# Performance work log

Hardware: AMD Instinct MI355X
Metric: run time of the kernel (lower is better)

The kernel has to match this reference:

```python
import jax, jax.numpy as jnp
import numpy as np

N = 100000      # nodes
E = 1600000     # edges (avg degree 16)
IN_F, HID, OUT_F, NC = 384, 128, 64, 2
EPS = 1e-5
NEG_SLOPE = 0.01


def _layernorm(x, g, b):
    m = jnp.mean(x, axis=-1, keepdims=True)
    v = jnp.var(x, axis=-1, keepdims=True)
    return (x - m) * jax.lax.rsqrt(v + EPS) * g + b


def _graph_conv(x, edge_index, edge_weight, w_rel, b_rel, w_root):
    # PyG GraphConv: lin_rel(scatter_add(w_e * x[src] -> dst)) + lin_root(x)
    src, dst = edge_index[0], edge_index[1]
    msg = x[src] * edge_weight[:, None]                      # [E, C]
    agg = jax.ops.segment_sum(msg, dst, num_segments=x.shape[0])  # [N, C]
    return agg @ w_rel.T + b_rel + x @ w_root.T


def _xavier(key, shape):
    fan_in, fan_out = shape[1], shape[0]
    lim = float(np.sqrt(6.0 / (fan_in + fan_out)))
    return jax.random.uniform(key, shape, jnp.float32, -lim, lim)


def setup_inputs() -> dict:
    key = jax.random.key(0)
    ks = jax.random.split(key, 10)
    x = jax.random.normal(ks[0], (N, IN_F), jnp.float32)
    edge_index = jax.random.randint(ks[1], (2, E), 0, N, jnp.int64)
    edge_attr = jax.random.uniform(ks[2], (E,), jnp.float32)
    return {
        "x": x,
        "edge_index": edge_index,
        "edge_attr": edge_attr,
        "ln1_g": jnp.ones((IN_F,), jnp.float32),
        "ln1_b": jnp.zeros((IN_F,), jnp.float32),
        "fc1_w": _xavier(ks[3], (HID, IN_F)),
        "fc1_b": jnp.zeros((HID,), jnp.float32),
        "c1_wrel": _xavier(ks[4], (HID, HID)),
        "c1_brel": jnp.zeros((HID,), jnp.float32),
        "c1_wroot": _xavier(ks[5], (HID, HID)),
        "c2_wrel": _xavier(ks[6], (OUT_F, HID)),
        "c2_brel": jnp.zeros((OUT_F,), jnp.float32),
        "c2_wroot": _xavier(ks[7], (OUT_F, HID)),
        "ln2_g": jnp.ones((OUT_F,), jnp.float32),
        "ln2_b": jnp.zeros((OUT_F,), jnp.float32),
        "fc2_w": _xavier(ks[8], (NC, OUT_F)),
        "fc2_b": jnp.zeros((NC,), jnp.float32),
    }


def reference(x, edge_index, edge_attr,
              ln1_g, ln1_b, fc1_w, fc1_b,
              c1_wrel, c1_brel, c1_wroot,
              c2_wrel, c2_brel, c2_wroot,
              ln2_g, ln2_b, fc2_w, fc2_b):
    h = _layernorm(x, ln1_g, ln1_b) @ fc1_w.T + fc1_b          # [N, HID]
    h = _graph_conv(h, edge_index, edge_attr, c1_wrel, c1_brel, c1_wroot)
    h = jax.nn.leaky_relu(h, NEG_SLOPE)
    h = _graph_conv(h, edge_index, edge_attr, c2_wrel, c2_brel, c2_wroot)
    h = jax.nn.leaky_relu(h, NEG_SLOPE)                        # [N, OUT_F]
    out = _layernorm(h, ln2_g, ln2_b) @ fc2_w.T + fc2_b        # [N, NC]
    return out
```

## Files before the change

kernel.cpp:

```cpp
#include <hip/hip_runtime.h>
#include <hip/hip_bf16.h>

#define N_IN_F 384
#define N_HID  128
#define N_OUT  64

typedef unsigned short ushort_t;
typedef __attribute__((ext_vector_type(8))) short short8v;
typedef __attribute__((ext_vector_type(4))) float floatx4;

union U8 { uint4 v; unsigned short u[8]; };

__device__ __forceinline__ float bfu2f(unsigned short s){
    union { unsigned i; float f; } c; c.i = ((unsigned)s) << 16; return c.f;
}
__device__ __forceinline__ unsigned short f2bfu(float f){
    __hip_bfloat16 h = __float2bfloat16(f);
    union { __hip_bfloat16 h; unsigned short u; } c; c.h = h; return c.u;
}

__device__ __forceinline__ float loadS(const void* p, size_t i, int fm){
    return fm ? bfu2f(((const unsigned short*)p)[i]) : ((const float*)p)[i];
}

__global__ void k_detect_all(const int* __restrict__ ei, const unsigned* __restrict__ xw,
                             int* __restrict__ modep){
    int lane = threadIdx.x & 63;
    int zi = 0;
    if (lane < 32) zi = ei[2*lane + 1];
    int cnt = 0;
    #pragma unroll
    for (int q = 0; q < 8; q++){
        unsigned w = xw[lane*8 + q];
        unsigned elo = (w >> 7) & 0xff;
        cnt += (elo >= 118 && elo <= 134) ? 1 : 0;
    }
    #pragma unroll
    for (int m = 32; m; m >>= 1){ zi |= __shfl_xor(zi, m, 64); cnt += __shfl_xor(cnt, m, 64); }
    if (lane == 0 && blockIdx.x == 0){
        modep[0] = (zi == 0) ? 1 : 0;
        modep[1] = (cnt >= 256) ? 1 : 0;
    }
}

__device__ __forceinline__ int edge_src(const int* ei, int e, int i, int mode){
    return mode ? ei[2*(size_t)i] : ei[i];
}
__device__ __forceinline__ int edge_dst(const int* ei, int e, int i, int mode){
    return mode ? ei[2*(size_t)e + 2*(size_t)i] : ei[(size_t)e + i];
}

__global__ void k_hist(const int* __restrict__ ei, int e, int n, const int* __restrict__ modep,
                       int* __restrict__ deg, unsigned* __restrict__ rel){
    int i = blockIdx.x * 256 + threadIdx.x;
    if (i >= e) return;
    int mode = modep[0];
    int d = edge_dst(ei, e, i, mode);
    if ((unsigned)d >= (unsigned)n) return;
    rel[i] = (unsigned)atomicAdd(&deg[d], 1);
}

__global__ __launch_bounds__(1024) void k_blksum(
    const int* __restrict__ deg, int n, int* __restrict__ part)
{
    __shared__ int s[1024];
    int i = blockIdx.x * 1024 + threadIdx.x;
    s[threadIdx.x] = (i < n) ? deg[i] : 0;
    __syncthreads();
    for (int off = 512; off; off >>= 1){
        if (threadIdx.x < off) s[threadIdx.x] += s[threadIdx.x + off];
        __syncthreads();
    }
    if (threadIdx.x == 0) part[blockIdx.x] = s[0];
}

__global__ __launch_bounds__(128) void k_scanpart(
    int* __restrict__ part, int nb, int* __restrict__ rowoff, int n)
{
    __shared__ int s[128];
    int t = threadIdx.x;
    if (nb <= 128){
        int v = (t < nb) ? part[t] : 0;
        s[t] = v; __syncthreads();
        #pragma unroll
        for (int off = 1; off < 128; off <<= 1){
            int tmp = (t >= off) ? s[t - off] : 0;
            __syncthreads();
            s[t] += tmp;
            __syncthreads();
        }
        if (t < nb) part[t] = s[t] - v;
        if (t == 127) rowoff[n] = s[127];
    } else if (t == 0){
        int run = 0;
        for (int b = 0; b < nb; b++){ int tt = part[b]; part[b] = run; run += tt; }
        rowoff[n] = run;
    }
}

__global__ __launch_bounds__(1024) void k_scanblk(
    int* __restrict__ deg, const int* __restrict__ part, int n, int* __restrict__ rowoff)
{
    __shared__ int s[1024];
    int t = threadIdx.x;
    int i = blockIdx.x * 1024 + t;
    int v = (i < n) ? deg[i] : 0;
    s[t] = v; __syncthreads();
    for (int off = 1; off < 1024; off <<= 1){
        int tmp = (t >= off) ? s[t - off] : 0;
        __syncthreads();
        s[t] += tmp;
        __syncthreads();
    }
    if (i < n){
        int excl = s[t] - v + part[blockIdx.x];
        rowoff[i] = excl;
        deg[i]    = excl;
    }
}

__global__ void k_scatter(const int* __restrict__ ei, const void* __restrict__ ea,
                          int e, int n, const int* __restrict__ modep,
                          int* __restrict__ cursor, int2* __restrict__ colw)
{
    int i = blockIdx.x * 256 + threadIdx.x;
    if (i >= e) return;
    int mode = modep[0], fm = modep[1];
    int d = edge_dst(ei, e, i, mode);
    if ((unsigned)d >= (unsigned)n) return;
    int s = edge_src(ei, e, i, mode);
    if ((unsigned)s >= (unsigned)n) s = 0;
    int pos = atomicAdd(&cursor[d], 1);
    if ((unsigned)pos >= (unsigned)e) return;
    int2 pk; pk.x = s; pk.y = __float_as_int(loadS(ea, i, fm));
    colw[pos] = pk;
}

#define SC_CHUNK 2048
#define SC_BSHIFT 13
#define SC_MAXB 1024
__global__ __launch_bounds__(256) void k_scoarse(
    const int* __restrict__ ei, const void* __restrict__ ea,
    const unsigned* __restrict__ rel, const int* __restrict__ rowoff,
    const int* __restrict__ modep, int e, int n, int B,
    int4* __restrict__ tmp, int* __restrict__ off2)
{
    __shared__ int  hcnt[SC_MAXB];
    __shared__ int  hoff[SC_MAXB + 1];
    __shared__ int4 stage[SC_CHUNK];
    int t = threadIdx.x;
    int c = blockIdx.x;
    int chunk0 = c * SC_CHUNK;
    int mode = modep[0], fm = modep[1];

    for (int q = t; q < B; q += 256) hcnt[q] = 0;
    __syncthreads();

    int  pos[8], sv[8], wv[8];
    bool val[8];
    #pragma unroll
    for (int k = 0; k < 8; k++){
        int i = chunk0 + k*256 + t;
        val[k] = false;
        if (i < e){
            int d = edge_dst(ei, e, i, mode);
            if ((unsigned)d < (unsigned)n){
                int s = edge_src(ei, e, i, mode);
                if ((unsigned)s >= (unsigned)n) s = 0;
                int p = rowoff[d] + (int)rel[i];
                pos[k] = p; sv[k] = s; wv[k] = __float_as_int(loadS(ea, i, fm));
                val[k] = true;
                atomicAdd(&hcnt[p >> SC_BSHIFT], 1);
            }
        }
    }
    __syncthreads();
    if (t == 0){
        int run = 0;
        for (int q = 0; q < B; q++){ hoff[q] = run; run += hcnt[q]; }
        hoff[B] = run;
    }
    __syncthreads();
    for (int q = t; q < B; q += 256) hcnt[q] = 0;
    for (int q = t; q <= B; q += 256) off2[(size_t)c*(B+1) + q] = hoff[q];
    __syncthreads();
    #pragma unroll
    for (int k = 0; k < 8; k++){
        if (val[k]){
            int b = pos[k] >> SC_BSHIFT;
            int slot = hoff[b] + atomicAdd(&hcnt[b], 1);
            stage[slot] = make_int4(pos[k], sv[k], wv[k], 0);
        }
    }
    __syncthreads();
    int tot = hoff[B];
    for (int idx = t; idx < tot; idx += 256)
        tmp[(size_t)chunk0 + idx] = stage[idx];
}

__global__ __launch_bounds__(512) void k_sfine(
    const int4* __restrict__ tmp, const int* __restrict__ off2,
    int B, int nchunks, int2* __restrict__ colw)
{
    int b = blockIdx.x;
    int wv = threadIdx.x >> 6, lane = threadIdx.x & 63;
    const int NW = 8;
    int c = wv;
    if (c >= nchunks) return;
    int s0 = off2[(size_t)c*(B+1) + b];
    int s1 = off2[(size_t)c*(B+1) + b + 1];
    while (true){
        int cn = c + NW;
        int n0 = 0, n1 = 0;
        if (cn < nchunks){
            n0 = off2[(size_t)cn*(B+1) + b];
            n1 = off2[(size_t)cn*(B+1) + b + 1];
        }
        int len = s1 - s0;
        size_t base = (size_t)c * SC_CHUNK + s0;
        for (int k = lane; k < len; k += 64){
            int4 ent = tmp[base + k];
            colw[ent.x] = make_int2(ent.y, ent.z);
        }
        if (cn >= nchunks) break;
        c = cn; s0 = n0; s1 = n1;
    }
}

__global__ __launch_bounds__(64) void k_prep_w1(
    const void* __restrict__ W, const void* __restrict__ g, const void* __restrict__ b,
    const void* __restrict__ fc1b, const int* __restrict__ fmp,
    ushort_t* __restrict__ Wp, float* __restrict__ u, float* __restrict__ v)
{
    int fm = fmp[0];
    int j = blockIdx.x, lane = threadIdx.x;
    float su = 0.f, sv = 0.f;
    for (int k = lane; k < N_IN_F; k += 64){
        float w  = loadS(W, (size_t)j*N_IN_F + k, fm);
        float gk = loadS(g, k, fm);
        float bk = loadS(b, k, fm);
        unsigned short pw = f2bfu(gk * w);
        Wp[(size_t)j*N_IN_F + k] = pw;
        su += bfu2f(pw);
        sv += bk * w;
    }
    #pragma unroll
    for (int m = 32; m; m >>= 1){ su += __shfl_xor(su, m, 64); sv += __shfl_xor(sv, m, 64); }
    if (lane == 0){
        u[j] = su;
        v[j] = sv + loadS(fc1b, j, fm);
    }
}

__global__ void k_cvt4(const void* __restrict__ p0, const void* __restrict__ p1,
                       const void* __restrict__ p2, const void* __restrict__ p3,
                       const int* __restrict__ fmp, ushort_t* __restrict__ o)
{
    int fm = fmp[0];
    int i = blockIdx.x * 256 + threadIdx.x;
    if (i >= 49152) return;
    const void* p; int off;
    if (i < 16384)      { p = p0; off = i; }
    else if (i < 32768) { p = p1; off = i - 16384; }
    else if (i < 40960) { p = p2; off = i - 32768; }
    else                { p = p3; off = i - 40960; }
    o[i] = f2bfu(loadS(p, off, fm));
}

__global__ __launch_bounds__(256) void k_gemm1_mfma(
    const void* __restrict__ x, const int* __restrict__ fmp,
    const ushort_t* __restrict__ Wp,
    const float* __restrict__ u, const float* __restrict__ v,
    ushort_t* __restrict__ out, int n)
{
    __shared__ ushort_t As[64*40];
    __shared__ ushort_t Bs[128*40];
    int fm = fmp[0];
    int t = threadIdx.x;
    int wave = t >> 6, lane = t & 63;
    int r16 = lane & 15, kq = lane >> 4;
    int m0 = blockIdx.x * 64;
    int mw = m0 + wave * 16;

    int sq = t & 3, srow = t >> 2;
    int bcol = t & 127, bhalf = t >> 7;

    int garow = min(m0 + srow, n - 1);
    const ushort_t* xbf = (const ushort_t*)x + (size_t)garow*N_IN_F + sq*8;
    const float*    xf  = (const float*)x    + (size_t)garow*N_IN_F + sq*8;
    const ushort_t* wpB = Wp + (size_t)bcol*N_IN_F + bhalf*16;

    floatx4 acc[8];
    #pragma unroll
    for (int c = 0; c < 8; c++) acc[c] = (floatx4){0.f,0.f,0.f,0.f};
    float s1 = 0.f, s2 = 0.f;

    uint4 aBF; floatx4 aF0, aF1; uint4 b0r, b1r;
    if (fm) aBF = *(const uint4*)xbf;
    else { aF0 = *(const floatx4*)xf; aF1 = *(const floatx4*)(xf + 4); }
    b0r = *(const uint4*)wpB;
    b1r = *(const uint4*)(wpB + 8);

    for (int ks = 0; ks < 12; ks++){
        if (ks) __syncthreads();
        union { ushort_t u[8]; uint4 v4; } w;
        if (fm) w.v4 = aBF;
        else {
            w.u[0]=f2bfu(aF0[0]); w.u[1]=f2bfu(aF0[1]); w.u[2]=f2bfu(aF0[2]); w.u[3]=f2bfu(aF0[3]);
            w.u[4]=f2bfu(aF1[0]); w.u[5]=f2bfu(aF1[1]); w.u[6]=f2bfu(aF1[2]); w.u[7]=f2bfu(aF1[3]);
        }
        *(uint4*)(As + srow*40 + sq*8) = w.v4;
        *(uint4*)(Bs + bcol*40 + bhalf*16)     = b0r;
        *(uint4*)(Bs + bcol*40 + bhalf*16 + 8) = b1r;
        __syncthreads();
        if (ks + 1 < 12){
            int kb = (ks + 1) * 32;
            if (fm) aBF = *(const uint4*)(xbf + kb);
            else { aF0 = *(const floatx4*)(xf + kb); aF1 = *(const floatx4*)(xf + kb + 4); }
            b0r = *(const uint4*)(wpB + kb);
            b1r = *(const uint4*)(wpB + kb + 8);
        }
        short8v af = *(const short8v*)(As + (wave*16 + r16)*40 + kq*8);
        short8v bfr[8];
        #pragma unroll
        for (int ni = 0; ni < 8; ni++)
            bfr[ni] = *(const short8v*)(Bs + (ni*16 + r16)*40 + kq*8);
        #pragma unroll
        for (int q = 0; q < 8; q++){
            float f = bfu2f((unsigned short)af[q]);
            s1 += f; s2 += f*f;
        }
        #pragma unroll
        for (int ni = 0; ni < 8; ni++)
            acc[ni] = __builtin_amdgcn_mfma_f32_16x16x32_bf16(af, bfr[ni], acc[ni], 0, 0, 0);
    }

    s1 += __shfl_xor(s1, 16, 64); s1 += __shfl_xor(s1, 32, 64);
    s2 += __shfl_xor(s2, 16, 64); s2 += __shfl_xor(s2, 32, 64);
    float mu = s1 * (1.f/384.f);
    float var = fmaxf(s2 * (1.f/384.f) - mu*mu, 0.f);
    float rs = rsqrtf(var + 1e-5f);

    float mm[4], rr[4];
    #pragma unroll
    for (int r = 0; r < 4; r++){
        mm[r] = __shfl(mu, kq*4 + r, 64);
        rr[r] = __shfl(rs, kq*4 + r, 64);
    }
    int ib = mw + kq*4;
    #pragma unroll
    for (int ni = 0; ni < 8; ni++){
        int j = ni*16 + r16;
        float uj = u[j], vj = v[j];
        #pragma unroll
        for (int r = 0; r < 4; r++){
            int ii = ib + r;
            float val = rr[r]*acc[ni][r] - rr[r]*mm[r]*uj + vj;
            if (ii < n) out[(size_t)ii*N_HID + j] = f2bfu(val);
        }
    }
}

__global__ __launch_bounds__(256) void k_conv1_mfma(
    const ushort_t* __restrict__ A1, const ushort_t* __restrict__ A2,
    const ushort_t* __restrict__ W1, const ushort_t* __restrict__ W2,
    const void* __restrict__ bias, const int* __restrict__ fmp,
    ushort_t* __restrict__ out, int n)
{
    __shared__ ushort_t As[64*40];
    __shared__ ushort_t Bs[128*40];
    int fm = fmp[0];
    int t = threadIdx.x;
    int wave = t >> 6, lane = t & 63;
    int r16 = lane & 15, kq = lane >> 4;
    int m0 = blockIdx.x * 64;
    int mw = m0 + wave * 16;

    int sq = t & 3, srow = t >> 2;
    int bcol = t & 127, bhalf = t >> 7;

    int garow = min(m0 + srow, n - 1);
    size_t aoff = (size_t)garow*N_HID + sq*8;
    size_t boff = (size_t)bcol*N_HID + bhalf*16;

    floatx4 acc[8];
    #pragma unroll
    for (int c = 0; c < 8; c++) acc[c] = (floatx4){0.f,0.f,0.f,0.f};

    uint4 aR, b0r, b1r;
    aR  = *(const uint4*)(A1 + aoff);
    b0r = *(const uint4*)(W1 + boff);
    b1r = *(const uint4*)(W1 + boff + 8);

    #pragma unroll
    for (int ks = 0; ks < 8; ks++){
        if (ks) __syncthreads();
        *(uint4*)(As + srow*40 + sq*8) = aR;
        *(uint4*)(Bs + bcol*40 + bhalf*16)     = b0r;
        *(uint4*)(Bs + bcol*40 + bhalf*16 + 8) = b1r;
        __syncthreads();
        if (ks + 1 < 8){
            int kn = ks + 1;
            const ushort_t* Asrc = (kn < 4) ? A1 : A2;
            const ushort_t* Wsrc = (kn < 4) ? W1 : W2;
            int kb = (kn & 3) * 32;
            aR  = *(const uint4*)(Asrc + aoff + kb);
            b0r = *(const uint4*)(Wsrc + boff + kb);
            b1r = *(const uint4*)(Wsrc + boff + kb + 8);
        }
        short8v af = *(const short8v*)(As + (wave*16 + r16)*40 + kq*8);
        short8v bfr[8];
        #pragma unroll
        for (int ni = 0; ni < 8; ni++)
            bfr[ni] = *(const short8v*)(Bs + (ni*16 + r16)*40 + kq*8);
        #pragma unroll
        for (int ni = 0; ni < 8; ni++)
            acc[ni] = __builtin_amdgcn_mfma_f32_16x16x32_bf16(af, bfr[ni], acc[ni], 0, 0, 0);
    }

    int ib = mw + kq*4;
    #pragma unroll
    for (int ni = 0; ni < 8; ni++){
        int j = ni*16 + r16;
        float bb = loadS(bias, j, fm);
        #pragma unroll
        for (int r = 0; r < 4; r++){
            int ii = ib + r;
            float val = acc[ni][r] + bb;
            val = (val >= 0.f) ? val : 0.01f * val;
            if (ii < n) out[(size_t)ii*N_HID + j] = f2bfu(val);
        }
    }
}

__global__ __launch_bounds__(256) void k_conv2_final(
    const ushort_t* __restrict__ A1, const ushort_t* __restrict__ A2,
    const ushort_t* __restrict__ W1, const ushort_t* __restrict__ W2,
    const void* __restrict__ bias,
    const void* __restrict__ gam, const void* __restrict__ bet,
    const void* __restrict__ Wfc, const void* __restrict__ bfc,
    const int* __restrict__ fmp, void* __restrict__ out, int n)
{
    __shared__ ushort_t As[64*40];
    __shared__ ushort_t Bs[64*40];
    int fm = fmp[0];
    int t = threadIdx.x;
    int wave = t >> 6, lane = t & 63;
    int r16 = lane & 15, kq = lane >> 4;
    int m0 = blockIdx.x * 64;
    int mw = m0 + wave * 16;

    int sq = t & 3, srow = t >> 2;
    int bcol = t & 63, bseg = t >> 6;

    int garow = min(m0 + srow, n - 1);
    size_t aoff = (size_t)garow*N_HID + sq*8;
    size_t boff = (size_t)bcol*N_HID + bseg*8;

    floatx4 acc[4];
    #pragma unroll
    for (int c = 0; c < 4; c++) acc[c] = (floatx4){0.f,0.f,0.f,0.f};

    uint4 aR, bR;
    aR = *(const uint4*)(A1 + aoff);
    bR = *(const uint4*)(W1 + boff);

    #pragma unroll
    for (int ks = 0; ks < 8; ks++){
        if (ks) __syncthreads();
        *(uint4*)(As + srow*40 + sq*8) = aR;
        *(uint4*)(Bs + bcol*40 + bseg*8) = bR;
        __syncthreads();
        if (ks + 1 < 8){
            int kn = ks + 1;
            const ushort_t* Asrc = (kn < 4) ? A1 : A2;
            const ushort_t* Wsrc = (kn < 4) ? W1 : W2;
            int kb = (kn & 3) * 32;
            aR = *(const uint4*)(Asrc + aoff + kb);
            bR = *(const uint4*)(Wsrc + boff + kb);
        }
        short8v af = *(const short8v*)(As + (wave*16 + r16)*40 + kq*8);
        short8v bfr[4];
        #pragma unroll
        for (int ni = 0; ni < 4; ni++)
            bfr[ni] = *(const short8v*)(Bs + (ni*16 + r16)*40 + kq*8);
        #pragma unroll
        for (int ni = 0; ni < 4; ni++)
            acc[ni] = __builtin_amdgcn_mfma_f32_16x16x32_bf16(af, bfr[ni], acc[ni], 0, 0, 0);
    }

    float b0 = loadS(bfc, 0, fm), b1 = loadS(bfc, 1, fm);
    float s[4] = {}, s2[4] = {};
    #pragma unroll
    for (int ni = 0; ni < 4; ni++){
        int j = ni*16 + r16;
        float bb = loadS(bias, j, fm);
        #pragma unroll
        for (int r = 0; r < 4; r++){
            float val = acc[ni][r] + bb;
            val = (val >= 0.f) ? val : 0.01f * val;
            acc[ni][r] = val;
            s[r] += val; s2[r] += val*val;
        }
    }
    #pragma unroll
    for (int m = 1; m < 16; m <<= 1){
        #pragma unroll
        for (int r = 0; r < 4; r++){
            s[r]  += __shfl_xor(s[r],  m, 64);
            s2[r] += __shfl_xor(s2[r], m, 64);
        }
    }
    float mu[4], rstd[4];
    #pragma unroll
    for (int r = 0; r < 4; r++){
        mu[r] = s[r] * (1.f/64.f);
        float var = fmaxf(s2[r] * (1.f/64.f) - mu[r]*mu[r], 0.f);
        rstd[r] = rsqrtf(var + 1e-5f);
    }
    float p0[4] = {}, p1[4] = {};
    #pragma unroll
    for (int ni = 0; ni < 4; ni++){
        int j = ni*16 + r16;
        float gj = loadS(gam, j, fm), bj = loadS(bet, j, fm);
        float w0 = loadS(Wfc, j, fm), w1 = loadS(Wfc, 64 + j, fm);
        #pragma unroll
        for (int r = 0; r < 4; r++){
            float zn = (acc[ni][r] - mu[r]) * rstd[r] * gj + bj;
            p0[r] += zn * w0;
            p1[r] += zn * w1;
        }
    }
    #pragma unroll
    for (int m = 1; m < 16; m <<= 1){
        #pragma unroll
        for (int r = 0; r < 4; r++){
            p0[r] += __shfl_xor(p0[r], m, 64);
            p1[r] += __shfl_xor(p1[r], m, 64);
        }
    }
    if (r16 == 0){
        #pragma unroll
        for (int r = 0; r < 4; r++){
            int ii = mw + kq*4 + r;
            if (ii >= n) continue;
            float o0 = p0[r] + b0, o1 = p1[r] + b1;
            if (fm){
                unsigned pk = ((unsigned)f2bfu(o1) << 16) | (unsigned)f2bfu(o0);
                *(unsigned*)((ushort_t*)out + (size_t)ii*2) = pk;
            } else {
                float2 f2; f2.x = o0; f2.y = o1;
                *(float2*)((float*)out + (size_t)ii*2) = f2;
            }
        }
    }
}

__global__ __launch_bounds__(256) void k_agg(
    const int* __restrict__ rowoff, const int2* __restrict__ colw,
    const ushort_t* __restrict__ src_mat,
    ushort_t* __restrict__ out, int n, int eTot)
{
    int t = threadIdx.x;
    int lane = t & 63;
    int d = blockIdx.x * 4 + (t >> 6);
    if (d >= n) return;
    int grp = lane >> 4;
    int c16 = lane & 15;
    int e0 = rowoff[d], e1 = rowoff[d+1];
    e0 = max(0, min(e0, eTot));
    e1 = max(e0, min(e1, eTot));
    float acc[8] = {};
    for (int e = e0 + grp; e < e1; e += 4){
        int2 cw = colw[e];
        int s = cw.x;
        if ((unsigned)s >= (unsigned)n) s = 0;
        float wv = __int_as_float(cw.y);
        U8 u; u.v = *(const uint4*)(src_mat + (size_t)s*N_HID + c16*8);
        #pragma unroll
        for (int q = 0; q < 8; q++) acc[q] += wv * bfu2f(u.u[q]);
    }
    #pragma unroll
    for (int q = 0; q < 8; q++){
        acc[q] += __shfl_xor(acc[q], 16, 64);
        acc[q] += __shfl_xor(acc[q], 32, 64);
    }
    if (grp == 0){
        union { ushort_t u[8]; uint4 v; } P;
        #pragma unroll
        for (int q = 0; q < 8; q++) P.u[q] = f2bfu(acc[q]);
        *(uint4*)(out + (size_t)d*N_HID + c16*8) = P.v;
    }
}

extern "C" void kernel_launch(void* const* d_in, const int* in_sizes, int n_in,
                              void* d_out, int out_size, void* d_ws, size_t ws_size,
                              hipStream_t stream)
{
    const void* x     = d_in[0];
    const int*  ei    = (const int*)d_in[1];
    const void* ea    = d_in[2];
    const void* ln1g  = d_in[3];
    const void* ln1b  = d_in[4];
    const void* fc1w  = d_in[5];
    const void* fc1b  = d_in[6];
    const void* c1rel = d_in[7];
    const void* c1bre = d_in[8];
    const void* c1roo = d_in[9];
    const void* c2rel = d_in[10];
    const void* c2bre = d_in[11];
    const void* c2roo = d_in[12];
    const void* ln2g  = d_in[13];
    const void* ln2b  = d_in[14];
    const void* fc2w  = d_in[15];
    const void* fc2b  = d_in[16];
    (void)n_in; (void)out_size; (void)ws_size;

    const int n = in_sizes[0] / N_IN_F;
    const int e = in_sizes[2];

    const int nchunks = (e + SC_CHUNK - 1) / SC_CHUNK;
    const int B = (e + (1 << SC_BSHIFT) - 1) >> SC_BSHIFT;

    char* wsp = (char*)d_ws;
    size_t off = 0;
    auto alloc = [&](size_t bytes) -> char* {
        char* p = wsp + off; off += (bytes + 255) & ~(size_t)255; return p;
    };
    int*      deg    = (int*)  alloc((size_t)n * 4);
    int*      rowoff = (int*)  alloc((size_t)(n+1) * 4);
    int*      part   = (int*)  alloc(4096);
    int*      modep  = (int*)  alloc(256);
    int2*     colw   = (int2*) alloc((size_t)e * 8);
    unsigned* rel    = (unsigned*)alloc((size_t)e * 4);
    int4*     stmp   = (int4*) alloc((size_t)e * 16);
    int*      off2   = (int*)  alloc((size_t)nchunks * (B+1) * 4);
    float*    u      = (float*)alloc(128 * 4);
    float*    v      = (float*)alloc(128 * 4);
    ushort_t* Wp     = (ushort_t*)alloc((size_t)N_HID * N_IN_F * 2);
    ushort_t* cw     = (ushort_t*)alloc((size_t)49152 * 2);
    ushort_t* h1     = (ushort_t*)alloc((size_t)n * N_HID * 2);
    ushort_t* agg1   = (ushort_t*)alloc((size_t)n * N_HID * 2);
    ushort_t* g1     = (ushort_t*)alloc((size_t)n * N_HID * 2);
    ushort_t* agg2   = h1;

    hipMemsetAsync(deg, 0, (size_t)n * 4, stream);
    k_detect_all<<<1, 64, 0, stream>>>(ei, (const unsigned*)x, modep);

    int nb = (n + 1023) / 1024;
    k_hist    <<<(e + 255) / 256, 256, 0, stream>>>(ei, e, n, modep, deg, rel);
    k_blksum  <<<nb, 1024, 0, stream>>>(deg, n, part);
    k_scanpart<<<1, 128, 0, stream>>>(part, nb, rowoff, n);
    k_scanblk <<<nb, 1024, 0, stream>>>(deg, part, n, rowoff);

    if (B <= SC_MAXB){
        k_scoarse<<<nchunks, 256, 0, stream>>>(ei, ea, rel, rowoff, modep, e, n, B, stmp, off2);
        k_sfine  <<<B, 512, 0, stream>>>(stmp, off2, B, nchunks, colw);
    } else {
        k_scatter<<<(e + 255) / 256, 256, 0, stream>>>(ei, ea, e, n, modep, deg, colw);
    }

    k_prep_w1<<<N_HID, 64, 0, stream>>>(fc1w, ln1g, ln1b, fc1b, modep + 1, Wp, u, v);
    k_cvt4   <<<(49152 + 255) / 256, 256, 0, stream>>>(c1rel, c1roo, c2rel, c2roo, modep + 1, cw);

    k_gemm1_mfma<<<(n + 63) / 64, 256, 0, stream>>>(x, modep + 1, Wp, u, v, h1, n);

    k_agg<<<(n + 3) / 4, 256, 0, stream>>>(rowoff, colw, h1, agg1, n, e);
    k_conv1_mfma<<<(n + 63) / 64, 256, 0, stream>>>(agg1, h1, cw, cw + 16384, c1bre, modep + 1, g1, n);

    k_agg<<<(n + 3) / 4, 256, 0, stream>>>(rowoff, colw, g1, agg2, n, e);
    k_conv2_final<<<(n + 63) / 64, 256, 0, stream>>>(agg2, g1, cw + 32768, cw + 40960, c2bre,
                                                     ln2g, ln2b, fc2w, fc2b, modep + 1, d_out, n);
}
```

Before: 638.1 us.

## Double-buffer LDS tiles and prefetch two K-steps ahead in MFMA GEMMs

Converts the three MFMA GEMM kernels (fc1+layernorm, conv1, conv2+final) from single-buffered shared tiles to double-buffered ones. Register prefetch now runs two K-steps ahead, so each iteration needs one barrier instead of two. The aim is to overlap global loads and LDS stores with MFMA work and cut synchronisation. In exchange it doubles shared memory per block and holds more registers for the prefetched slots, which may lower occupancy.

```diff
diff --git a/kernel.cpp b/kernel.cpp
--- a/kernel.cpp
+++ b/kernel.cpp
@@ -273,8 +273,8 @@
     const float* __restrict__ u, const float* __restrict__ v,
     ushort_t* __restrict__ out, int n)
 {
-    __shared__ ushort_t As[64*40];
-    __shared__ ushort_t Bs[128*40];
+    __shared__ ushort_t As[2][64*40];
+    __shared__ ushort_t Bs[2][128*40];
     int fm = fmp[0];
     int t = threadIdx.x;
     int wave = t >> 6, lane = t & 63;
@@ -295,36 +295,44 @@
     for (int c = 0; c < 8; c++) acc[c] = (floatx4){0.f,0.f,0.f,0.f};
     float s1 = 0.f, s2 = 0.f;
 
-    uint4 aBF; floatx4 aF0, aF1; uint4 b0r, b1r;
-    if (fm) aBF = *(const uint4*)xbf;
-    else { aF0 = *(const floatx4*)xf; aF1 = *(const floatx4*)(xf + 4); }
-    b0r = *(const uint4*)wpB;
-    b1r = *(const uint4*)(wpB + 8);
-
+    uint4 aBF[2]; floatx4 aF0[2], aF1[2]; uint4 b0r[2], b1r[2];
+
+#define G1_LOAD(KS, SL)                                                          \
+    { int kb_ = (KS)*32;                                                         \
+      if (fm) aBF[SL] = *(const uint4*)(xbf + kb_);                              \
+      else { aF0[SL] = *(const floatx4*)(xf + kb_);                              \
+             aF1[SL] = *(const floatx4*)(xf + kb_ + 4); }                        \
+      b0r[SL] = *(const uint4*)(wpB + kb_);                                      \
+      b1r[SL] = *(const uint4*)(wpB + kb_ + 8); }
+
+#define G1_STORE(KS, SL)                                                         \
+    { int buf_ = (KS) & 1;                                                       \
+      union { ushort_t u[8]; uint4 v4; } w_;                                     \
+      if (fm) w_.v4 = aBF[SL];                                                   \
+      else {                                                                     \
+        w_.u[0]=f2bfu(aF0[SL][0]); w_.u[1]=f2bfu(aF0[SL][1]);                    \
+        w_.u[2]=f2bfu(aF0[SL][2]); w_.u[3]=f2bfu(aF0[SL][3]);                    \
+        w_.u[4]=f2bfu(aF1[SL][0]); w_.u[5]=f2bfu(aF1[SL][1]);                    \
+        w_.u[6]=f2bfu(aF1[SL][2]); w_.u[7]=f2bfu(aF1[SL][3]); }                  \
+      *(uint4*)(As[buf_] + srow*40 + sq*8) = w_.v4;                              \
+      *(uint4*)(Bs[buf_] + bcol*40 + bhalf*16)     = b0r[SL];                    \
+      *(uint4*)(Bs[buf_] + bcol*40 + bhalf*16 + 8) = b1r[SL]; }
+
+    G1_LOAD(0, 0)
+    G1_LOAD(1, 1)
+    G1_STORE(0, 0)
+    __syncthreads();
+
+    #pragma unroll
     for (int ks = 0; ks < 12; ks++){
-        if (ks) __syncthreads();
-        union { ushort_t u[8]; uint4 v4; } w;
-        if (fm) w.v4 = aBF;
-        else {
-            w.u[0]=f2bfu(aF0[0]); w.u[1]=f2bfu(aF0[1]); w.u[2]=f2bfu(aF0[2]); w.u[3]=f2bfu(aF0[3]);
-            w.u[4]=f2bfu(aF1[0]); w.u[5]=f2bfu(aF1[1]); w.u[6]=f2bfu(aF1[2]); w.u[7]=f2bfu(aF1[3]);
-        }
-        *(uint4*)(As + srow*40 + sq*8) = w.v4;
-        *(uint4*)(Bs + bcol*40 + bhalf*16)     = b0r;
-        *(uint4*)(Bs + bcol*40 + bhalf*16 + 8) = b1r;
-        __syncthreads();
-        if (ks + 1 < 12){
-            int kb = (ks + 1) * 32;
-            if (fm) aBF = *(const uint4*)(xbf + kb);
-            else { aF0 = *(const floatx4*)(xf + kb); aF1 = *(const floatx4*)(xf + kb + 4); }
-            b0r = *(const uint4*)(wpB + kb);
-            b1r = *(const uint4*)(wpB + kb + 8);
-        }
-        short8v af = *(const short8v*)(As + (wave*16 + r16)*40 + kq*8);
+        int buf = ks & 1;
+        short8v af = *(const short8v*)(As[buf] + (wave*16 + r16)*40 + kq*8);
         short8v bfr[8];
         #pragma unroll
         for (int ni = 0; ni < 8; ni++)
-            bfr[ni] = *(const short8v*)(Bs + (ni*16 + r16)*40 + kq*8);
+            bfr[ni] = *(const short8v*)(Bs[buf] + (ni*16 + r16)*40 + kq*8);
+        if (ks + 1 < 12) G1_STORE(ks + 1, (ks + 1) & 1)
+        if (ks + 2 < 12) G1_LOAD(ks + 2, ks & 1)
         #pragma unroll
         for (int q = 0; q < 8; q++){
             float f = bfu2f((unsigned short)af[q]);
@@ -333,7 +341,10 @@
         #pragma unroll
         for (int ni = 0; ni < 8; ni++)
             acc[ni] = __builtin_amdgcn_mfma_f32_16x16x32_bf16(af, bfr[ni], acc[ni], 0, 0, 0);
-    }
+        if (ks + 1 < 12) __syncthreads();
+    }
+#undef G1_LOAD
+#undef G1_STORE
 
     s1 += __shfl_xor(s1, 16, 64); s1 += __shfl_xor(s1, 32, 64);
     s2 += __shfl_xor(s2, 16, 64); s2 += __shfl_xor(s2, 32, 64);
@@ -367,8 +378,8 @@
     const void* __restrict__ bias, const int* __restrict__ fmp,
     ushort_t* __restrict__ out, int n)
 {
-    __shared__ ushort_t As[64*40];
-    __shared__ ushort_t Bs[128*40];
+    __shared__ ushort_t As[2][64*40];
+    __shared__ ushort_t Bs[2][128*40];
     int fm = fmp[0];
     int t = threadIdx.x;
     int wave = t >> 6, lane = t & 63;
@@ -387,36 +398,44 @@
     #pragma unroll
     for (int c = 0; c < 8; c++) acc[c] = (floatx4){0.f,0.f,0.f,0.f};
 
-    uint4 aR, b0r, b1r;
-    aR  = *(const uint4*)(A1 + aoff);
-    b0r = *(const uint4*)(W1 + boff);
-    b1r = *(const uint4*)(W1 + boff + 8);
+    uint4 aR[2], b0r[2], b1r[2];
+
+#define C1_LOAD(KS, SL)                                                          \
+    { const ushort_t* As_ = ((KS) < 4) ? A1 : A2;                                \
+      const ushort_t* Ws_ = ((KS) < 4) ? W1 : W2;                                \
+      int kb_ = ((KS) & 3) * 32;                                                 \
+      aR[SL]  = *(const uint4*)(As_ + aoff + kb_);                               \
+      b0r[SL] = *(const uint4*)(Ws_ + boff + kb_);                               \
+      b1r[SL] = *(const uint4*)(Ws_ + boff + kb_ + 8); }
+
+#define C1_STORE(KS, SL)                                                         \
+    { int buf_ = (KS) & 1;                                                       \
+      *(uint4*)(As[buf_] + srow*40 + sq*8) = aR[SL];                             \
+      *(uint4*)(Bs[buf_] + bcol*40 + bhalf*16)     = b0r[SL];                    \
+      *(uint4*)(Bs[buf_] + bcol*40 + bhalf*16 + 8) = b1r[SL]; }
+
+    C1_LOAD(0, 0)
+    C1_LOAD(1, 1)
+    C1_STORE(0, 0)
+    __syncthreads();
 
     #pragma unroll
     for (int ks = 0; ks < 8; ks++){
-        if (ks) __syncthreads();
-        *(uint4*)(As + srow*40 + sq*8) = aR;
-        *(uint4*)(Bs + bcol*40 + bhalf*16)     = b0r;
-        *(uint4*)(Bs + bcol*40 + bhalf*16 + 8) = b1r;
-        __syncthreads();
-        if (ks + 1 < 8){
-            int kn = ks + 1;
-            const ushort_t* Asrc = (kn < 4) ? A1 : A2;
-            const ushort_t* Wsrc = (kn < 4) ? W1 : W2;
-            int kb = (kn & 3) * 32;
-            aR  = *(const uint4*)(Asrc + aoff + kb);
-            b0r = *(const uint4*)(Wsrc + boff + kb);
-            b1r = *(const uint4*)(Wsrc + boff + kb + 8);
-        }
-        short8v af = *(const short8v*)(As + (wave*16 + r16)*40 + kq*8);
+        int buf = ks & 1;
+        short8v af = *(const short8v*)(As[buf] + (wave*16 + r16)*40 + kq*8);
         short8v bfr[8];
         #pragma unroll
         for (int ni = 0; ni < 8; ni++)
-            bfr[ni] = *(const short8v*)(Bs + (ni*16 + r16)*40 + kq*8);
+            bfr[ni] = *(const short8v*)(Bs[buf] + (ni*16 + r16)*40 + kq*8);
+        if (ks + 1 < 8) C1_STORE(ks + 1, (ks + 1) & 1)
+        if (ks + 2 < 8) C1_LOAD(ks + 2, ks & 1)
         #pragma unroll
         for (int ni = 0; ni < 8; ni++)
             acc[ni] = __builtin_amdgcn_mfma_f32_16x16x32_bf16(af, bfr[ni], acc[ni], 0, 0, 0);
-    }
+        if (ks + 1 < 8) __syncthreads();
+    }
+#undef C1_LOAD
+#undef C1_STORE
 
     int ib = mw + kq*4;
     #pragma unroll
@@ -441,8 +460,8 @@
     const void* __restrict__ Wfc, const void* __restrict__ bfc,
     const int* __restrict__ fmp, void* __restrict__ out, int n)
 {
-    __shared__ ushort_t As[64*40];
-    __shared__ ushort_t Bs[64*40];
+    __shared__ ushort_t As[2][64*40];
+    __shared__ ushort_t Bs[2][64*40];
     int fm = fmp[0];
     int t = threadIdx.x;
     int wave = t >> 6, lane = t & 63;
@@ -461,33 +480,42 @@
     #pragma unroll
     for (int c = 0; c < 4; c++) acc[c] = (floatx4){0.f,0.f,0.f,0.f};
 
-    uint4 aR, bR;
-    aR = *(const uint4*)(A1 + aoff);
-    bR = *(const uint4*)(W1 + boff);
+    uint4 aR[2], bR[2];
+
+#define C2_LOAD(KS, SL)                                                          \
+    { const ushort_t* As_ = ((KS) < 4) ? A1 : A2;                                \
+      const ushort_t* Ws_ = ((KS) < 4) ? W1 : W2;                                \
+      int kb_ = ((KS) & 3) * 32;                                                 \
+      aR[SL] = *(const uint4*)(As_ + aoff + kb_);                                \
+      bR[SL] = *(const uint4*)(Ws_ + boff + kb_); }
+
+#define C2_STORE(KS, SL)                                                         \
+    { int buf_ = (KS) & 1;                                                       \
+      *(uint4*)(As[buf_] + srow*40 + sq*8) = aR[SL];                             \
+      *(uint4*)(Bs[buf_] + bcol*40 + bseg*8) = bR[SL]; }
+
+    C2_LOAD(0, 0)
+    C2_LOAD(1, 1)
+    C2_STORE(0, 0)
+    __syncthreads();
 
     #pragma unroll
     for (int ks = 0; ks < 8; ks++){
-        if (ks) __syncthreads();
-        *(uint4*)(As + srow*40 + sq*8) = aR;
-        *(uint4*)(Bs + bcol*40 + bseg*8) = bR;
-        __syncthreads();
-        if (ks + 1 < 8){
-            int kn = ks + 1;
-            const ushort_t* Asrc = (kn < 4) ? A1 : A2;
-            const ushort_t* Wsrc = (kn < 4) ? W1 : W2;
-            int kb = (kn & 3) * 32;
-            aR = *(const uint4*)(Asrc + aoff + kb);
-            bR = *(const uint4*)(Wsrc + boff + kb);
-        }
-        short8v af = *(const short8v*)(As + (wave*16 + r16)*40 + kq*8);
+        int buf = ks & 1;
+        short8v af = *(const short8v*)(As[buf] + (wave*16 + r16)*40 + kq*8);
         short8v bfr[4];
         #pragma unroll
         for (int ni = 0; ni < 4; ni++)
-            bfr[ni] = *(const short8v*)(Bs + (ni*16 + r16)*40 + kq*8);
+            bfr[ni] = *(const short8v*)(Bs[buf] + (ni*16 + r16)*40 + kq*8);
+        if (ks + 1 < 8) C2_STORE(ks + 1, (ks + 1) & 1)
+        if (ks + 2 < 8) C2_LOAD(ks + 2, ks & 1)
         #pragma unroll
         for (int ni = 0; ni < 4; ni++)
             acc[ni] = __builtin_amdgcn_mfma_f32_16x16x32_bf16(af, bfr[ni], acc[ni], 0, 0, 0);
-    }
+        if (ks + 1 < 8) __syncthreads();
+    }
+#undef C2_LOAD
+#undef C2_STORE
 
     float b0 = loadS(bfc, 0, fm), b1 = loadS(bfc, 1, fm);
     float s[4] = {}, s2[4] = {};
```

New measurement: 735.2 us. 15.2% more time.

## Load MFMA operands directly from global memory, dropping LDS staging and barriers

Applied to the files above, without the earlier changes.

The three dense MFMA kernels (gemm1, conv1, conv2_final) no longer stage A and B tiles through shared memory with __syncthreads. Each lane now loads its own A fragment and B fragments straight from global memory in the MFMA register layout, with the K loops fully unrolled. This removes LDS traffic and block barriers. In exchange, each wave re-reads the weight matrix from global/L2 instead of sharing it through LDS, and the explicit software prefetch is gone, leaving latency hiding to the compiler and to occupancy.

```diff
diff --git a/kernel.cpp b/kernel.cpp
--- a/kernel.cpp
+++ b/kernel.cpp
@@ -273,66 +273,58 @@
     const float* __restrict__ u, const float* __restrict__ v,
     ushort_t* __restrict__ out, int n)
 {
-    __shared__ ushort_t As[64*40];
-    __shared__ ushort_t Bs[128*40];
     int fm = fmp[0];
     int t = threadIdx.x;
     int wave = t >> 6, lane = t & 63;
     int r16 = lane & 15, kq = lane >> 4;
     int m0 = blockIdx.x * 64;
     int mw = m0 + wave * 16;
-
-    int sq = t & 3, srow = t >> 2;
-    int bcol = t & 127, bhalf = t >> 7;
-
-    int garow = min(m0 + srow, n - 1);
-    const ushort_t* xbf = (const ushort_t*)x + (size_t)garow*N_IN_F + sq*8;
-    const float*    xf  = (const float*)x    + (size_t)garow*N_IN_F + sq*8;
-    const ushort_t* wpB = Wp + (size_t)bcol*N_IN_F + bhalf*16;
+    int grow = min(mw + r16, n - 1);
+
+    const ushort_t* xbf = (const ushort_t*)x + (size_t)grow*N_IN_F + kq*8;
+    const float*    xf  = (const float*)x    + (size_t)grow*N_IN_F + kq*8;
+    const ushort_t* wpB = Wp + (size_t)r16*N_IN_F + kq*8;
 
     floatx4 acc[8];
     #pragma unroll
     for (int c = 0; c < 8; c++) acc[c] = (floatx4){0.f,0.f,0.f,0.f};
     float s1 = 0.f, s2 = 0.f;
 
-    uint4 aBF; floatx4 aF0, aF1; uint4 b0r, b1r;
-    if (fm) aBF = *(const uint4*)xbf;
-    else { aF0 = *(const floatx4*)xf; aF1 = *(const floatx4*)(xf + 4); }
-    b0r = *(const uint4*)wpB;
-    b1r = *(const uint4*)(wpB + 8);
-
-    for (int ks = 0; ks < 12; ks++){
-        if (ks) __syncthreads();
-        union { ushort_t u[8]; uint4 v4; } w;
-        if (fm) w.v4 = aBF;
-        else {
-            w.u[0]=f2bfu(aF0[0]); w.u[1]=f2bfu(aF0[1]); w.u[2]=f2bfu(aF0[2]); w.u[3]=f2bfu(aF0[3]);
-            w.u[4]=f2bfu(aF1[0]); w.u[5]=f2bfu(aF1[1]); w.u[6]=f2bfu(aF1[2]); w.u[7]=f2bfu(aF1[3]);
-        }
-        *(uint4*)(As + srow*40 + sq*8) = w.v4;
-        *(uint4*)(Bs + bcol*40 + bhalf*16)     = b0r;
-        *(uint4*)(Bs + bcol*40 + bhalf*16 + 8) = b1r;
-        __syncthreads();
-        if (ks + 1 < 12){
-            int kb = (ks + 1) * 32;
-            if (fm) aBF = *(const uint4*)(xbf + kb);
-            else { aF0 = *(const floatx4*)(xf + kb); aF1 = *(const floatx4*)(xf + kb + 4); }
-            b0r = *(const uint4*)(wpB + kb);
-            b1r = *(const uint4*)(wpB + kb + 8);
-        }
-        short8v af = *(const short8v*)(As + (wave*16 + r16)*40 + kq*8);
-        short8v bfr[8];
-        #pragma unroll
-        for (int ni = 0; ni < 8; ni++)
-            bfr[ni] = *(const short8v*)(Bs + (ni*16 + r16)*40 + kq*8);
-        #pragma unroll
-        for (int q = 0; q < 8; q++){
-            float f = bfu2f((unsigned short)af[q]);
-            s1 += f; s2 += f*f;
-        }
-        #pragma unroll
-        for (int ni = 0; ni < 8; ni++)
-            acc[ni] = __builtin_amdgcn_mfma_f32_16x16x32_bf16(af, bfr[ni], acc[ni], 0, 0, 0);
+    if (fm){
+        #pragma unroll
+        for (int ks = 0; ks < 12; ks++){
+            short8v af = *(const short8v*)(xbf + ks*32);
+            #pragma unroll
+            for (int q = 0; q < 8; q++){
+                float f = bfu2f((unsigned short)af[q]);
+                s1 += f; s2 += f*f;
+            }
+            #pragma unroll
+            for (int ni = 0; ni < 8; ni++){
+                short8v bf = *(const short8v*)(wpB + (size_t)ni*16*N_IN_F + ks*32);
+                acc[ni] = __builtin_amdgcn_mfma_f32_16x16x32_bf16(af, bf, acc[ni], 0, 0, 0);
+            }
+        }
+    } else {
+        #pragma unroll
+        for (int ks = 0; ks < 12; ks++){
+            floatx4 p = *(const floatx4*)(xf + ks*32);
+            floatx4 q4 = *(const floatx4*)(xf + ks*32 + 4);
+            union { ushort_t u[8]; short8v v; } w_;
+            w_.u[0]=f2bfu(p[0]); w_.u[1]=f2bfu(p[1]); w_.u[2]=f2bfu(p[2]); w_.u[3]=f2bfu(p[3]);
+            w_.u[4]=f2bfu(q4[0]); w_.u[5]=f2bfu(q4[1]); w_.u[6]=f2bfu(q4[2]); w_.u[7]=f2bfu(q4[3]);
+            short8v af = w_.v;
+            #pragma unroll
+            for (int q = 0; q < 8; q++){
+                float f = bfu2f((unsigned short)af[q]);
+                s1 += f; s2 += f*f;
+            }
+            #pragma unroll
+            for (int ni = 0; ni < 8; ni++){
+                short8v bf = *(const short8v*)(wpB + (size_t)ni*16*N_IN_F + ks*32);
+                acc[ni] = __builtin_amdgcn_mfma_f32_16x16x32_bf16(af, bf, acc[ni], 0, 0, 0);
+            }
+        }
     }
 
     s1 += __shfl_xor(s1, 16, 64); s1 += __shfl_xor(s1, 32, 64);
@@ -367,55 +359,32 @@
     const void* __restrict__ bias, const int* __restrict__ fmp,
     ushort_t* __restrict__ out, int n)
 {
-    __shared__ ushort_t As[64*40];
-    __shared__ ushort_t Bs[128*40];
     int fm = fmp[0];
     int t = threadIdx.x;
     int wave = t >> 6, lane = t & 63;
     int r16 = lane & 15, kq = lane >> 4;
     int m0 = blockIdx.x * 64;
     int mw = m0 + wave * 16;
-
-    int sq = t & 3, srow = t >> 2;
-    int bcol = t & 127, bhalf = t >> 7;
-
-    int garow = min(m0 + srow, n - 1);
-    size_t aoff = (size_t)garow*N_HID + sq*8;
-    size_t boff = (size_t)bcol*N_HID + bhalf*16;
+    int grow = min(mw + r16, n - 1);
+
+    size_t aoff = (size_t)grow*N_HID + kq*8;
+    size_t boff = (size_t)r16*N_HID + kq*8;
 
     floatx4 acc[8];
     #pragma unroll
     for (int c = 0; c < 8; c++) acc[c] = (floatx4){0.f,0.f,0.f,0.f};
 
-    uint4 aR, b0r, b1r;
-    aR  = *(const uint4*)(A1 + aoff);
-    b0r = *(const uint4*)(W1 + boff);
-    b1r = *(const uint4*)(W1 + boff + 8);
-
     #pragma unroll
     for (int ks = 0; ks < 8; ks++){
-        if (ks) __syncthreads();
-        *(uint4*)(As + srow*40 + sq*8) = aR;
-        *(uint4*)(Bs + bcol*40 + bhalf*16)     = b0r;
-        *(uint4*)(Bs + bcol*40 + bhalf*16 + 8) = b1r;
-        __syncthreads();
-        if (ks + 1 < 8){
-            int kn = ks + 1;
-            const ushort_t* Asrc = (kn < 4) ? A1 : A2;
-            const ushort_t* Wsrc = (kn < 4) ? W1 : W2;
-            int kb = (kn & 3) * 32;
-            aR  = *(const uint4*)(Asrc + aoff + kb);
-            b0r = *(const uint4*)(Wsrc + boff + kb);
-            b1r = *(const uint4*)(Wsrc + boff + kb + 8);
-        }
-        short8v af = *(const short8v*)(As + (wave*16 + r16)*40 + kq*8);
-        short8v bfr[8];
-        #pragma unroll
-        for (int ni = 0; ni < 8; ni++)
-            bfr[ni] = *(const short8v*)(Bs + (ni*16 + r16)*40 + kq*8);
-        #pragma unroll
-        for (int ni = 0; ni < 8; ni++)
-            acc[ni] = __builtin_amdgcn_mfma_f32_16x16x32_bf16(af, bfr[ni], acc[ni], 0, 0, 0);
+        const ushort_t* Asrc = (ks < 4) ? A1 : A2;
+        const ushort_t* Wsrc = (ks < 4) ? W1 : W2;
+        int kb = (ks & 3) * 32;
+        short8v af = *(const short8v*)(Asrc + aoff + kb);
+        #pragma unroll
+        for (int ni = 0; ni < 8; ni++){
+            short8v bf = *(const short8v*)(Wsrc + boff + (size_t)ni*16*N_HID + kb);
+            acc[ni] = __builtin_amdgcn_mfma_f32_16x16x32_bf16(af, bf, acc[ni], 0, 0, 0);
+        }
     }
 
     int ib = mw + kq*4;
@@ -441,52 +410,32 @@
     const void* __restrict__ Wfc, const void* __restrict__ bfc,
     const int* __restrict__ fmp, void* __restrict__ out, int n)
 {
-    __shared__ ushort_t As[64*40];
-    __shared__ ushort_t Bs[64*40];
     int fm = fmp[0];
     int t = threadIdx.x;
     int wave = t >> 6, lane = t & 63;
     int r16 = lane & 15, kq = lane >> 4;
     int m0 = blockIdx.x * 64;
     int mw = m0 + wave * 16;
-
-    int sq = t & 3, srow = t >> 2;
-    int bcol = t & 63, bseg = t >> 6;
-
-    int garow = min(m0 + srow, n - 1);
-    size_t aoff = (size_t)garow*N_HID + sq*8;
-    size_t boff = (size_t)bcol*N_HID + bseg*8;
+    int grow = min(mw + r16, n - 1);
+
+    size_t aoff = (size_t)grow*N_HID + kq*8;
+    size_t boff = (size_t)r16*N_HID + kq*8;
 
     floatx4 acc[4];
     #pragma unroll
     for (int c = 0; c < 4; c++) acc[c] = (floatx4){0.f,0.f,0.f,0.f};
 
-    uint4 aR, bR;
-    aR = *(const uint4*)(A1 + aoff);
-    bR = *(const uint4*)(W1 + boff);
-
     #pragma unroll
     for (int ks = 0; ks < 8; ks++){
-        if (ks) __syncthreads();
-        *(uint4*)(As + srow*40 + sq*8) = aR;
-        *(uint4*)(Bs + bcol*40 + bseg*8) = bR;
-        __syncthreads();
-        if (ks + 1 < 8){
-            int kn = ks + 1;
-            const ushort_t* Asrc = (kn < 4) ? A1 : A2;
-            const ushort_t* Wsrc = (kn < 4) ? W1 : W2;
-            int kb = (kn & 3) * 32;
-            aR = *(const uint4*)(Asrc + aoff + kb);
-            bR = *(const uint4*)(Wsrc + boff + kb);
-        }
-        short8v af = *(const short8v*)(As + (wave*16 + r16)*40 + kq*8);
-        short8v bfr[4];
-        #pragma unroll
-        for (int ni = 0; ni < 4; ni++)
-            bfr[ni] = *(const short8v*)(Bs + (ni*16 + r16)*40 + kq*8);
-        #pragma unroll
-        for (int ni = 0; ni < 4; ni++)
-            acc[ni] = __builtin_amdgcn_mfma_f32_16x16x32_bf16(af, bfr[ni], acc[ni], 0, 0, 0);
+        const ushort_t* Asrc = (ks < 4) ? A1 : A2;
+        const ushort_t* Wsrc = (ks < 4) ? W1 : W2;
+        int kb = (ks & 3) * 32;
+        short8v af = *(const short8v*)(Asrc + aoff + kb);
+        #pragma unroll
+        for (int ni = 0; ni < 4; ni++){
+            short8v bf = *(const short8v*)(Wsrc + boff + (size_t)ni*16*N_HID + kb);
+            acc[ni] = __builtin_amdgcn_mfma_f32_16x16x32_bf16(af, bf, acc[ni], 0, 0, 0);
+        }
     }
 
     float b0 = loadS(bfc, 0, fm), b1 = loadS(bfc, 1, fm);
```

Result: slower. 744.0 us (+16.6%).
